# Performance work log

Measured on AMD Instinct MI355X. Metric: run time of the kernel, lower is better.

## Reference

```python
import jax, jax.numpy as jnp
import numpy as np

EMBED_DIM = 4096
LOW_RANK = 512
BATCH = 8192
K_SEL = 128


def setup_inputs() -> dict:
    key = jax.random.key(0)
    k1, k2, k3, k4 = jax.random.split(key, 4)
    base = jax.random.normal(k1, (BATCH, EMBED_DIM), dtype=jnp.float32)
    source = jax.random.normal(k2, (BATCH, EMBED_DIM), dtype=jnp.float32)
    # fast path: only subspaces[0] is used (all examples share the same index set)
    row = jax.random.randint(k3, (1, K_SEL), 0, LOW_RANK)
    subspaces = jnp.broadcast_to(row, (BATCH, K_SEL)).astype(jnp.int64)
    # orthogonal (column-orthonormal) rotation weight, as produced by
    # torch.nn.utils.parametrizations.orthogonal on [embed_dim, low_rank]
    W, _ = jnp.linalg.qr(jax.random.normal(k4, (EMBED_DIM, LOW_RANK), dtype=jnp.float32))
    return {"base": base, "source": source, "subspaces": subspaces, "W": W}


def reference(base, source, subspaces, W):
    # rotated_base / rotated_source: [B, r]
    # diff in rotated space, gather selected subspace columns, project back.
    sel = subspaces[0]                      # [k] shared index set (fast path)
    diff = (source - base) @ W              # [B, r]
    diff_sel = diff[:, sel]                 # [B, k]
    W_sel = W[:, sel]                       # [d, k]
    out = base + diff_sel @ W_sel.T         # [B, d]
    return out.astype(base.dtype)
```

## Files before the change

### kernel.cpp

```cpp
#include <hip/hip_runtime.h>
#include <hip/hip_bf16.h>

typedef __attribute__((ext_vector_type(4))) float  f32x4;
typedef __attribute__((ext_vector_type(8))) short  short8;
typedef unsigned int u32;

#define EMBED 4096
#define LR    512
#define KSEL  128
#define BATCH 8192

__device__ __forceinline__ short f2bf(float x) {
  union { float f; unsigned u; } c; c.f = x;
  unsigned r = c.u + 0x7FFFu + ((c.u >> 16) & 1u);
  return (short)(r >> 16);
}
__device__ __forceinline__ void gload16(const void* g, void* l) {
  __builtin_amdgcn_global_load_lds((const __attribute__((address_space(1))) u32*)g,
                                   (__attribute__((address_space(3))) u32*)l, 16, 0, 0);
}

__global__ __launch_bounds__(256) void pack_w_kernel(
    const float* __restrict__ W, const int* __restrict__ sel,
    short* __restrict__ Wp, short* __restrict__ Wtp) {
  int idx = blockIdx.x * 256 + threadIdx.x;
  int e = idx >> 7;
  int c = idx & 127;
  int r = sel[c];
  short v = f2bf(W[e * LR + r]);
  Wp [(((e >> 3) << 7) + c) * 8 + (e & 7)] = v;
  Wtp[(((c >> 3) << 12) + e) * 8 + (c & 7)] = v;
}

__global__ __launch_bounds__(256, 2) void gemm1_kernel(
    const float* __restrict__ base, const float* __restrict__ src,
    const short* __restrict__ Wp, short* __restrict__ Tp) {
  __shared__ __align__(16) char smem[65536];
  const int t  = threadIdx.x;
  const int w  = t >> 6, l = t & 63;
  const int lr = l & 15, lg = l >> 4;
  const int row0 = blockIdx.x * 16;

  const int srow = t >> 6;
  const int sc   = t & 63;

  #define STAGE(s, b) do {                                                  \
    char* d_ = smem + (b) * 32768 + t * 16;                                 \
    _Pragma("unroll")                                                       \
    for (int i = 0; i < 4; ++i) {                                           \
      const int row = i * 4 + srow;                                         \
      const size_t go = (size_t)(row0 + row) * EMBED + (s) * 256            \
                        + ((sc ^ (row & 7)) << 2);                          \
      gload16(base + go, d_ + i * 4096);                                    \
      gload16(src  + go, d_ + 16384 + i * 4096);                            \
    }                                                                       \
  } while (0)

  const short8* wq = (const short8*)Wp;
  f32x4 acc0 = {0.f, 0.f, 0.f, 0.f}, acc1 = {0.f, 0.f, 0.f, 0.f};

  STAGE(0, 0);
  int b = 0;
  for (int s = 0; s < 16; ++s) {
    __syncthreads();
    const int kc = s * 256;
    short8 bf[16];
    #pragma unroll
    for (int kstep = 0; kstep < 8; ++kstep) {
      const int kg = ((kc + kstep * 32) >> 3) + lg;
      bf[kstep * 2]     = wq[(size_t)kg * 128 + w * 32 + lr];
      bf[kstep * 2 + 1] = wq[(size_t)kg * 128 + w * 32 + 16 + lr];
    }
    if (s < 15) STAGE(s + 1, b ^ 1);
    const char* tb = smem + b * 32768 + lr * 1024;
    #pragma unroll
    for (int kstep = 0; kstep < 8; ++kstep) {
      const int j0 = (kstep * 8 + lg * 2)     ^ (lr & 7);
      const int j1 = (kstep * 8 + lg * 2 + 1) ^ (lr & 7);
      f32x4 b0 = *(const f32x4*)(tb + j0 * 16);
      f32x4 b1 = *(const f32x4*)(tb + j1 * 16);
      f32x4 s0 = *(const f32x4*)(tb + 16384 + j0 * 16);
      f32x4 s1 = *(const f32x4*)(tb + 16384 + j1 * 16);
      union { short8 v; __hip_bfloat162 h[4]; } u;
      u.h[0] = __float22bfloat162_rn(make_float2(s0[0] - b0[0], s0[1] - b0[1]));
      u.h[1] = __float22bfloat162_rn(make_float2(s0[2] - b0[2], s0[3] - b0[3]));
      u.h[2] = __float22bfloat162_rn(make_float2(s1[0] - b1[0], s1[1] - b1[1]));
      u.h[3] = __float22bfloat162_rn(make_float2(s1[2] - b1[2], s1[3] - b1[3]));
      acc0 = __builtin_amdgcn_mfma_f32_16x16x32_bf16(u.v, bf[kstep * 2],     acc0, 0, 0, 0);
      acc1 = __builtin_amdgcn_mfma_f32_16x16x32_bf16(u.v, bf[kstep * 2 + 1], acc1, 0, 0, 0);
    }
    b ^= 1;
  }
  #undef STAGE

  #pragma unroll
  for (int ct = 0; ct < 2; ++ct) {
    f32x4 a = ct ? acc1 : acc0;
    const int kk = w * 32 + ct * 16 + lr;
    short* dst = Tp + (size_t)(((kk >> 3) << 13) + row0 + (lg << 2)) * 8 + (kk & 7);
    #pragma unroll
    for (int r = 0; r < 4; ++r) dst[r * 8] = f2bf(a[r]);
  }
}

__global__ __launch_bounds__(256) void gemm2_kernel(
    const float* __restrict__ base, const short* __restrict__ Tp,
    const short* __restrict__ Wtp, float* __restrict__ out) {
  const int t  = threadIdx.x;
  const int w  = t >> 6, l = t & 63;
  const int lr = l & 15, lg = l >> 4;
  const int mt = blockIdx.x >> 4, nt = blockIdx.x & 15;
  const int row0 = mt * 64;
  const int col0 = nt * 256 + w * 64;

  short8 afr[4][4];
  #pragma unroll
  for (int m = 0; m < 4; ++m)
    #pragma unroll
    for (int ks = 0; ks < 4; ++ks)
      afr[m][ks] = *(const short8*)(Tp + (size_t)(((ks * 4 + lg) << 13) + row0 + m * 16 + lr) * 8);

  f32x4 acc[4][4];
  #pragma unroll
  for (int m = 0; m < 4; ++m)
    #pragma unroll
    for (int nf = 0; nf < 4; ++nf) acc[m][nf] = (f32x4){0.f, 0.f, 0.f, 0.f};

  #pragma unroll
  for (int nf = 0; nf < 4; ++nf) {
    short8 bfr[4];
    #pragma unroll
    for (int ks = 0; ks < 4; ++ks)
      bfr[ks] = *(const short8*)(Wtp + (size_t)(((ks * 4 + lg) << 12) + col0 + nf * 16 + lr) * 8);
    #pragma unroll
    for (int m = 0; m < 4; ++m)
      #pragma unroll
      for (int ks = 0; ks < 4; ++ks)
        acc[m][nf] = __builtin_amdgcn_mfma_f32_16x16x32_bf16(afr[m][ks], bfr[ks], acc[m][nf], 0, 0, 0);
  }

  #pragma unroll
  for (int m = 0; m < 4; ++m)
    #pragma unroll
    for (int r = 0; r < 4; ++r) {
      const size_t row = row0 + m * 16 + lg * 4 + r;
      #pragma unroll
      for (int nf = 0; nf < 4; ++nf) {
        const size_t o = row * EMBED + col0 + nf * 16 + lr;
        out[o] = base[o] + acc[m][nf][r];
      }
    }
}

extern "C" void kernel_launch(void* const* d_in, const int* in_sizes, int n_in,
                              void* d_out, int out_size, void* d_ws, size_t ws_size,
                              hipStream_t stream) {
  const float* base = (const float*)d_in[0];
  const float* src  = (const float*)d_in[1];
  const int*   sub  = (const int*)d_in[2];
  const float* W    = (const float*)d_in[3];
  float* out = (float*)d_out;

  short* Wp  = (short*)d_ws;
  short* Wtp = Wp  + EMBED * KSEL;
  short* Tp  = Wtp + EMBED * KSEL;

  pack_w_kernel<<<EMBED * KSEL / 256, 256, 0, stream>>>(W, sub, Wp, Wtp);
  gemm1_kernel<<<BATCH / 16, 256, 0, stream>>>(base, src, Wp, Tp);
  gemm2_kernel<<<(BATCH / 64) * 16, 256, 0, stream>>>(base, Tp, Wtp, out);
}
```

Baseline: 135.0 us.

## Precompute bf16 difference in separate pass before first GEMM

Adds a streaming kernel that computes source minus base, converts it to bf16 and writes it to workspace. A new first-GEMM kernel then reads the half-size bf16 operand with a smaller LDS footprint and higher occupancy, instead of loading two fp32 tiles per stage. The aim is to separate the bandwidth-bound elementwise step from the MFMA loop. The cost is an extra 64MB write and read plus another launch. The new path only runs when the workspace is large enough, otherwise the fused kernel is kept.

```diff
diff --git a/kernel.cpp b/kernel.cpp
--- a/kernel.cpp
+++ b/kernel.cpp
@@ -32,6 +32,85 @@
   Wtp[(((c >> 3) << 12) + e) * 8 + (c & 7)] = v;
 }
 
+__global__ __launch_bounds__(256) void diff_kernel(
+    const float* __restrict__ base, const float* __restrict__ src,
+    short* __restrict__ Dp) {
+  const size_t nchunks = (size_t)BATCH * EMBED / 8;
+  const size_t stride  = (size_t)gridDim.x * 256;
+  for (size_t i = (size_t)blockIdx.x * 256 + threadIdx.x; i < nchunks; i += stride) {
+    const float* b = base + i * 8;
+    const float* s = src  + i * 8;
+    f32x4 b0 = *(const f32x4*)b;
+    f32x4 b1 = *(const f32x4*)(b + 4);
+    f32x4 s0 = *(const f32x4*)s;
+    f32x4 s1 = *(const f32x4*)(s + 4);
+    union { short8 v; __hip_bfloat162 h[4]; } u;
+    u.h[0] = __float22bfloat162_rn(make_float2(s0[0] - b0[0], s0[1] - b0[1]));
+    u.h[1] = __float22bfloat162_rn(make_float2(s0[2] - b0[2], s0[3] - b0[3]));
+    u.h[2] = __float22bfloat162_rn(make_float2(s1[0] - b1[0], s1[1] - b1[1]));
+    u.h[3] = __float22bfloat162_rn(make_float2(s1[2] - b1[2], s1[3] - b1[3]));
+    *(short8*)(Dp + i * 8) = u.v;
+  }
+}
+
+__global__ __launch_bounds__(256, 3) void gemm1b_kernel(
+    const short* __restrict__ Dp, const short* __restrict__ Wp,
+    short* __restrict__ Tp) {
+  __shared__ __align__(16) char smem[16384];
+  const int t  = threadIdx.x;
+  const int w  = t >> 6, l = t & 63;
+  const int lr = l & 15, lg = l >> 4;
+  const int row0 = blockIdx.x * 16;
+
+  const int r0 = t >> 5,         c0 = t & 31;
+  const int r1 = (t + 256) >> 5, c1 = t & 31;
+  const short* g0 = Dp + (size_t)(row0 + r0) * EMBED + ((c0 ^ (r0 & 7)) << 3);
+  const short* g1 = Dp + (size_t)(row0 + r1) * EMBED + ((c1 ^ (r1 & 7)) << 3);
+
+  #define STAGE(s, b) do {                        \
+    char* d_ = smem + (b) * 8192 + t * 16;        \
+    gload16(g0 + (s) * 256, d_);                  \
+    gload16(g1 + (s) * 256, d_ + 4096);           \
+  } while (0)
+
+  const short8* wq = (const short8*)Wp;
+  f32x4 acc0 = {0.f, 0.f, 0.f, 0.f}, acc1 = {0.f, 0.f, 0.f, 0.f};
+
+  STAGE(0, 0);
+  int b = 0;
+  for (int s = 0; s < 16; ++s) {
+    __syncthreads();
+    const int kc = s * 256;
+    short8 bf[16];
+    #pragma unroll
+    for (int kstep = 0; kstep < 8; ++kstep) {
+      const int kg = ((kc + kstep * 32) >> 3) + lg;
+      bf[kstep * 2]     = wq[(size_t)kg * 128 + w * 32 + lr];
+      bf[kstep * 2 + 1] = wq[(size_t)kg * 128 + w * 32 + 16 + lr];
+    }
+    if (s < 15) STAGE(s + 1, b ^ 1);
+    const char* tb = smem + b * 8192 + lr * 512;
+    #pragma unroll
+    for (int kstep = 0; kstep < 8; ++kstep) {
+      const int c = (kstep * 4 + lg) ^ (lr & 7);
+      short8 a = *(const short8*)(tb + c * 16);
+      acc0 = __builtin_amdgcn_mfma_f32_16x16x32_bf16(a, bf[kstep * 2],     acc0, 0, 0, 0);
+      acc1 = __builtin_amdgcn_mfma_f32_16x16x32_bf16(a, bf[kstep * 2 + 1], acc1, 0, 0, 0);
+    }
+    b ^= 1;
+  }
+  #undef STAGE
+
+  #pragma unroll
+  for (int ct = 0; ct < 2; ++ct) {
+    f32x4 a = ct ? acc1 : acc0;
+    const int kk = w * 32 + ct * 16 + lr;
+    short* dst = Tp + (size_t)(((kk >> 3) << 13) + row0 + (lg << 2)) * 8 + (kk & 7);
+    #pragma unroll
+    for (int r = 0; r < 4; ++r) dst[r * 8] = f2bf(a[r]);
+  }
+}
+
 __global__ __launch_bounds__(256, 2) void gemm1_kernel(
     const float* __restrict__ base, const float* __restrict__ src,
     const short* __restrict__ Wp, short* __restrict__ Tp) {
@@ -40,7 +119,6 @@
   const int w  = t >> 6, l = t & 63;
   const int lr = l & 15, lg = l >> 4;
   const int row0 = blockIdx.x * 16;
-
   const int srow = t >> 6;
   const int sc   = t & 63;
 
@@ -164,8 +242,17 @@
   short* Wp  = (short*)d_ws;
   short* Wtp = Wp  + EMBED * KSEL;
   short* Tp  = Wtp + EMBED * KSEL;
+  short* Dp  = Tp  + BATCH * KSEL;
 
   pack_w_kernel<<<EMBED * KSEL / 256, 256, 0, stream>>>(W, sub, Wp, Wtp);
-  gemm1_kernel<<<BATCH / 16, 256, 0, stream>>>(base, src, Wp, Tp);
+
+  const size_t need = (size_t)4 * 1024 * 1024 + (size_t)BATCH * EMBED * 2;
+  if (ws_size >= need) {
+    diff_kernel<<<2048, 256, 0, stream>>>(base, src, Dp);
+    gemm1b_kernel<<<BATCH / 16, 256, 0, stream>>>(Dp, Wp, Tp);
+  } else {
+    gemm1_kernel<<<BATCH / 16, 256, 0, stream>>>(base, src, Wp, Tp);
+  }
+
   gemm2_kernel<<<(BATCH / 64) * 16, 256, 0, stream>>>(base, Tp, Wtp, out);
 }
```

After: 158.8 us. +17.6%, slower.
